# Kernel tuning notes

Hardware: AMD Instinct MI355X
Metric: run time of the kernel (lower is better)

Reference implementation:

```python
import jax, jax.numpy as jnp
import numpy as np

B, D, T = 8, 1024, 2048          # batch, input_dim, time
CD, CS = 256, 8192               # codebook_dim, codebook_size


def _wn_weight(v, g):
    # torch weight_norm for Conv1d(k=1): weight = g * v / ||v|| with norm over
    # all dims except the output-channel dim. v: (out, in), g: (out, 1).
    return g * v / jnp.linalg.norm(v, axis=1, keepdims=True)


def setup_inputs() -> dict:
    key = jax.random.key(0)
    k0, k1, k2, k3 = jax.random.split(key, 4)
    z = jax.random.normal(k0, (B, D, T), dtype=jnp.float32)
    # in_proj: WNConv1d(input_dim -> codebook_dim, k=1)
    in_v = jax.random.normal(k1, (CD, D), dtype=jnp.float32) * 0.02
    in_g = jnp.ones((CD, 1), dtype=jnp.float32)
    in_b = jnp.zeros((CD,), dtype=jnp.float32)
    # out_proj: WNConv1d(codebook_dim -> input_dim, k=1)
    out_v = jax.random.normal(k2, (D, CD), dtype=jnp.float32) * 0.02
    out_g = jnp.ones((D, 1), dtype=jnp.float32)
    out_b = jnp.zeros((D,), dtype=jnp.float32)
    codebook = jax.random.normal(k3, (CS, CD), dtype=jnp.float32)
    return {"z": z, "in_v": in_v, "in_g": in_g, "in_b": in_b,
            "out_v": out_v, "out_g": out_g, "out_b": out_b,
            "codebook": codebook}


def reference(z, in_v, in_g, in_b, out_v, out_g, out_b, codebook):
    # in_proj (1x1 conv == per-timestep linear): (B, D, T) -> (B, CD, T)
    w_in = _wn_weight(in_v, in_g)
    z_e = jnp.einsum('bdt,cd->bct', z, w_in) + in_b[None, :, None]

    # flatten to (N, CD), N = B*T
    enc = z_e.transpose(0, 2, 1).reshape(-1, z_e.shape[1])

    # squared euclidean cdist via GEMM: ||e||^2 - 2 e.c^T + ||c||^2
    dist = (jnp.sum(enc * enc, axis=1, keepdims=True)
            - 2.0 * enc @ codebook.T
            + jnp.sum(codebook * codebook, axis=1)[None, :])  # (N, CS)

    indices = jnp.argmax(-dist, axis=1).reshape(z.shape[0], -1)  # (B, T)

    # decode_code: embedding gather then channels-first: (B, CD, T)
    z_q_code = codebook[indices].transpose(0, 2, 1)

    # out_proj: (B, CD, T) -> (B, D, T)
    w_out = _wn_weight(out_v, out_g)
    z_q = jnp.einsum('bct,dc->bdt', z_q_code, w_out) + out_b[None, :, None]
    return z_q, indices, z_e
```

## Files before the change

kernel.cpp:

```cpp
#include <hip/hip_runtime.h>
#include <math.h>

#define B_  8
#define D_  1024
#define T_  2048
#define CD_ 256
#define CS_ 8192
#define N_  (B_*T_)

#define NSPLIT 8
#define CODES_PER_SPLIT (CS_/NSPLIT)
#define NT_SPLIT (CODES_PER_SPLIT/64)
#define DELTA 1.5f

#define ROWS_PER_WAVE 64
#define SCAN_ROWS 256
#define TILE_CODES 64

#define WS_ZEN   0
#define WS_CBB   2097152
#define WS_WH    (WS_CBB + 1048576)
#define WS_WM    (WS_WH + 131072)
#define WS_WL    (WS_WM + 131072)
#define WS_WOB   (WS_WL + 131072)
#define WS_C2    (WS_WOB + 131072)
#define WS_CNT   (WS_C2 + CS_)
#define WS_CAND  (WS_CNT + N_)
#define WS_IDX   (WS_CAND + N_*16)

#define OUT_ZQ  0
#define OUT_IDX (B_*D_*T_)
#define OUT_ZE  (OUT_IDX + B_*T_)

using short8v = __attribute__((ext_vector_type(8))) short;
using float4v = __attribute__((ext_vector_type(4))) float;

__device__ __forceinline__ float wave_sum64(float v) {
#pragma unroll
  for (int off = 32; off >= 1; off >>= 1) v += __shfl_xor(v, off);
  return v;
}

__device__ __forceinline__ unsigned short f2bf_rne(float f) {
  unsigned int u = __float_as_uint(f);
  u += 0x7fffu + ((u >> 16) & 1u);
  return (unsigned short)(u >> 16);
}

__device__ __forceinline__ float bf2f(unsigned short u) {
  return __uint_as_float(((unsigned)u) << 16);
}

__device__ __forceinline__ void gload_lds16(const void* g, void* l) {
  __builtin_amdgcn_global_load_lds(
      (const __attribute__((address_space(1))) void*)g,
      (__attribute__((address_space(3))) void*)l, 16, 0, 0);
}

__global__ __launch_bounds__(256) void prep_all(
    const float* __restrict__ in_v, const float* __restrict__ in_g,
    const float* __restrict__ out_v, const float* __restrict__ out_g,
    const float* __restrict__ cb,
    unsigned short* __restrict__ wh, unsigned short* __restrict__ wm,
    unsigned short* __restrict__ wl, unsigned short* __restrict__ wob,
    float* __restrict__ c2, unsigned short* __restrict__ cbb) {
  __shared__ float sh[4];
  int blk = blockIdx.x, tid = threadIdx.x;
  if (blk < CD_) {
    int c = blk;
    float v[4]; float s = 0.f;
#pragma unroll
    for (int i = 0; i < 4; ++i) {
      v[i] = in_v[c * D_ + tid + 256 * i];
      s = fmaf(v[i], v[i], s);
    }
    s = wave_sum64(s);
    if ((tid & 63) == 0) sh[tid >> 6] = s;
    __syncthreads();
    float tot = sh[0] + sh[1] + sh[2] + sh[3];
    float scale = in_g[c] / sqrtf(tot);
#pragma unroll
    for (int i = 0; i < 4; ++i) {
      int d = tid + 256 * i;
      float x = v[i] * scale;
      unsigned short h = f2bf_rne(x);
      float r1 = x - bf2f(h);
      unsigned short m = (unsigned short)(__float_as_uint(r1) >> 16);
      float r2 = r1 - bf2f(m);
      unsigned short lo = (unsigned short)(__float_as_uint(r2) >> 16);
      wh[c * D_ + d] = h; wm[c * D_ + d] = m; wl[c * D_ + d] = lo;
    }
  } else if (blk < CD_ + D_) {
    int d = blk - CD_;
    float v = out_v[d * CD_ + tid];
    float s = wave_sum64(v * v);
    if ((tid & 63) == 0) sh[tid >> 6] = s;
    __syncthreads();
    float tot = sh[0] + sh[1] + sh[2] + sh[3];
    float scale = out_g[d] / sqrtf(tot);
    wob[d * CD_ + tid] = f2bf_rne(v * scale);
  } else if (blk < CD_ + D_ + CS_ / 4) {
    int w = tid >> 6, lane = tid & 63;
    int s = (blk - CD_ - D_) * 4 + w;
    float acc = 0.f;
#pragma unroll
    for (int i = 0; i < 4; ++i) {
      float v = cb[(size_t)s * CD_ + lane + 64 * i];
      acc = fmaf(v, v, acc);
    }
    acc = wave_sum64(acc);
    if (lane == 0) c2[s] = acc;
  } else {
    size_t i = (size_t)(blk - CD_ - D_ - CS_ / 4) * 256 + tid;
    float4 v0 = *(const float4*)&cb[i * 8];
    float4 v1 = *(const float4*)&cb[i * 8 + 4];
    float f[8] = {v0.x, v0.y, v0.z, v0.w, v1.x, v1.y, v1.z, v1.w};
    unsigned short us[8];
#pragma unroll
    for (int m = 0; m < 8; ++m) us[m] = f2bf_rne(f[m]);
    *(uint4*)&cbb[i * 8] = *(uint4*)&us[0];
  }
}

__global__ __launch_bounds__(256, 2) void ze_mfma(
    const float* __restrict__ z,
    const unsigned short* __restrict__ whp, const unsigned short* __restrict__ wmp,
    const unsigned short* __restrict__ wlp, const float* __restrict__ in_b,
    float* __restrict__ out, unsigned short* __restrict__ zeN) {
  __shared__ __align__(16) char zbuf[2][16 * 1040];
  __shared__ __align__(16) unsigned short abuf[2][3][2048];
  int tid = threadIdx.x;
  int w = tid >> 6, l = tid & 63;
  int lrow = l & 15, lg = l >> 4;
  int t0 = blockIdx.x * 128, c0 = blockIdx.y * 64, b = blockIdx.z;
  const float* zb = z + (size_t)b * D_ * T_;
  char* zbuf_b = &zbuf[0][0];
  char* abuf_b = (char*)&abuf[0][0][0];

  auto stage = [&](int buf, int kc) {
#pragma unroll
    for (int i = 0; i < 4; ++i) {
      int g = w * 4 + i;
      int row = 2 * g + (l >> 5);
      gload_lds16(&zb[(size_t)(kc + row) * T_ + t0 + (l & 31) * 4],
                  zbuf_b + buf * 16640 + g * 1040);
    }
    int c = w * 16 + (l >> 2);
    int doff = (l & 3) * 8;
    gload_lds16(&whp[(size_t)(c0 + c) * D_ + kc + doff],
                abuf_b + buf * 12288 + w * 1024);
    gload_lds16(&wmp[(size_t)(c0 + c) * D_ + kc + doff],
                abuf_b + buf * 12288 + 4096 + w * 1024);
    gload_lds16(&wlp[(size_t)(c0 + c) * D_ + kc + doff],
                abuf_b + buf * 12288 + 8192 + w * 1024);
  };

  float4v acc[4][2];
#pragma unroll
  for (int rf = 0; rf < 4; ++rf)
#pragma unroll
    for (int cf = 0; cf < 2; ++cf) acc[rf][cf] = (float4v){0.f, 0.f, 0.f, 0.f};

  stage(0, 0);
  int cur = 0;
  for (int kt = 0; kt < D_ / 32; ++kt) {
    if (kt + 1 < D_ / 32) {
      stage(cur ^ 1, (kt + 1) * 32);
      asm volatile("s_waitcnt vmcnt(7)" ::: "memory");
    } else {
      asm volatile("s_waitcnt vmcnt(0)" ::: "memory");
    }
    __builtin_amdgcn_sched_barrier(0);
    __builtin_amdgcn_s_barrier();

    short8v bh[2], bm[2], bl[2];
#pragma unroll
    for (int cf = 0; cf < 2; ++cf) {
      const char* zp = zbuf_b + cur * 16640 + lg * 4160 +
                       (w * 32 + cf * 16 + lrow) * 4;
      float x[8];
#pragma unroll
      for (int j = 0; j < 8; ++j)
        x[j] = *(const float*)(zp + (j >> 1) * 1040 + (j & 1) * 512);
      __align__(16) unsigned short h8[8], m8[8], l8[8];
#pragma unroll
      for (int j = 0; j < 8; ++j) {
        unsigned short h = f2bf_rne(x[j]);
        float r1 = x[j] - bf2f(h);
        unsigned short m = (unsigned short)(__float_as_uint(r1) >> 16);
        float r2 = r1 - bf2f(m);
        unsigned short lo = (unsigned short)(__float_as_uint(r2) >> 16);
        h8[j] = h; m8[j] = m; l8[j] = lo;
      }
      bh[cf] = *(const short8v*)h8;
      bm[cf] = *(const short8v*)m8;
      bl[cf] = *(const short8v*)l8;
    }
    short8v ah[4], am[4], al[4];
#pragma unroll
    for (int rf = 0; rf < 4; ++rf) {
      int coff = (rf * 16 + lrow) * 64 + lg * 16;
      const char* ab = abuf_b + cur * 12288 + coff;
      ah[rf] = *(const short8v*)(ab);
      am[rf] = *(const short8v*)(ab + 4096);
      al[rf] = *(const short8v*)(ab + 8192);
    }
#pragma unroll
    for (int rf = 0; rf < 4; ++rf)
#pragma unroll
      for (int cf = 0; cf < 2; ++cf) {
        float4v a_ = acc[rf][cf];
        a_ = __builtin_amdgcn_mfma_f32_16x16x32_bf16(ah[rf], bh[cf], a_, 0, 0, 0);
        a_ = __builtin_amdgcn_mfma_f32_16x16x32_bf16(am[rf], bh[cf], a_, 0, 0, 0);
        a_ = __builtin_amdgcn_mfma_f32_16x16x32_bf16(ah[rf], bm[cf], a_, 0, 0, 0);
        a_ = __builtin_amdgcn_mfma_f32_16x16x32_bf16(am[rf], bm[cf], a_, 0, 0, 0);
        a_ = __builtin_amdgcn_mfma_f32_16x16x32_bf16(al[rf], bh[cf], a_, 0, 0, 0);
        a_ = __builtin_amdgcn_mfma_f32_16x16x32_bf16(ah[rf], bl[cf], a_, 0, 0, 0);
        acc[rf][cf] = a_;
      }
    __builtin_amdgcn_s_barrier();
    cur ^= 1;
  }

  int tbase = t0 + w * 32;
#pragma unroll
  for (int rf = 0; rf < 4; ++rf) {
    float bv[4];
#pragma unroll
    for (int rg = 0; rg < 4; ++rg) bv[rg] = in_b[c0 + rf * 16 + lg * 4 + rg];
#pragma unroll
    for (int cf = 0; cf < 2; ++cf) {
      int t = tbase + cf * 16 + lrow;
#pragma unroll
      for (int rg = 0; rg < 4; ++rg) {
        int c = c0 + rf * 16 + lg * 4 + rg;
        out[OUT_ZE + (size_t)(b * CD_ + c) * T_ + t] = acc[rf][cf][rg] + bv[rg];
      }
      __align__(8) unsigned short us[4];
#pragma unroll
      for (int rg = 0; rg < 4; ++rg) us[rg] = f2bf_rne(acc[rf][cf][rg] + bv[rg]);
      *(uint2*)&zeN[(size_t)(b * T_ + t) * CD_ + c0 + rf * 16 + lg * 4] =
          *(uint2*)us;
    }
  }
}

template <int COLLECT>
__global__ __launch_bounds__(256, 2) void vq_scan(
    const unsigned short* __restrict__ zeN, const unsigned short* __restrict__ cbb,
    const float* __restrict__ c2, float* __restrict__ bestq,
    int* __restrict__ cnt, int* __restrict__ cand) {
  __shared__ __align__(16) unsigned short smem[2][TILE_CODES * CD_];
  int tid = threadIdx.x;
  int w = tid >> 6, l = tid & 63;
  int lrow = l & 15, lg = l >> 4;
  int rowbase = blockIdx.x * SCAN_ROWS + w * ROWS_PER_WAVE;
  int cq = blockIdx.y;
  int cbase0 = cq * CODES_PER_SPLIT;

  if (COLLECT == 0 && cq == 0)
    cnt[blockIdx.x * SCAN_ROWS + tid] = 0;

  short8v a[4][8];
#pragma unroll
  for (int rf = 0; rf < 4; ++rf)
#pragma unroll
    for (int ks = 0; ks < 8; ++ks)
      a[rf][ks] = *(const short8v*)&zeN[((size_t)(rowbase + rf * 16 + lrow)) * CD_ + ks * 32 + lg * 8];

  float best[16];
  float thr[16];
#pragma unroll
  for (int s = 0; s < 16; ++s) best[s] = -3.4e38f;
  if (COLLECT) {
#pragma unroll
    for (int s = 0; s < 16; ++s) {
      int rf = s >> 2, rg = s & 3;
      thr[s] = bestq[rowbase + rf * 16 + lg * 4 + rg];
    }
  }

  int lhalf = l >> 5;
  int lcol = (l & 31) * 16;
  char* smem_b = (char*)&smem[0][0];
  const char* cbb_b = (const char*)cbb;
  int xsw = (lrow & 7) << 4;

  auto stage = [&](int buf, int cbase) {
#pragma unroll
    for (int r = 0; r < 8; ++r) {
      int code = w * 16 + r * 2 + lhalf;
      size_t goff = (size_t)(cbase + code) * 512 + (size_t)(lcol ^ ((code & 7) << 4));
      gload_lds16(cbb_b + goff, smem_b + buf * 32768 + (w * 8 + r) * 1024);
    }
  };

  stage(0, cbase0);

  for (int t = 0; t < NT_SPLIT; ++t) {
    int buf = t & 1;
    int cbase = cbase0 + t * TILE_CODES;

    float hc2[4];
#pragma unroll
    for (int cf = 0; cf < 4; ++cf) hc2[cf] = 0.5f * c2[cbase + cf * 16 + lrow];

    if (t + 1 < NT_SPLIT) {
      stage(buf ^ 1, cbase + TILE_CODES);
      asm volatile("s_waitcnt vmcnt(8)" ::: "memory");
    } else {
      asm volatile("s_waitcnt vmcnt(0)" ::: "memory");
    }
    __builtin_amdgcn_sched_barrier(0);
    __builtin_amdgcn_s_barrier();

    const char* bufb = smem_b + buf * 32768;
#pragma unroll
    for (int cf = 0; cf < 4; ++cf) {
      const char* bbase = bufb + (cf * 16 + lrow) * 512;
      float4v acc[4];
#pragma unroll
      for (int rf = 0; rf < 4; ++rf) acc[rf] = (float4v){0.f, 0.f, 0.f, 0.f};
#pragma unroll
      for (int ks = 0; ks < 8; ++ks) {
        short8v bfrag = *(const short8v*)(bbase + ((ks * 64 + lg * 16) ^ xsw));
        acc[0] = __builtin_amdgcn_mfma_f32_16x16x32_bf16(a[0][ks], bfrag, acc[0], 0, 0, 0);
        acc[1] = __builtin_amdgcn_mfma_f32_16x16x32_bf16(a[1][ks], bfrag, acc[1], 0, 0, 0);
        acc[2] = __builtin_amdgcn_mfma_f32_16x16x32_bf16(a[2][ks], bfrag, acc[2], 0, 0, 0);
        acc[3] = __builtin_amdgcn_mfma_f32_16x16x32_bf16(a[3][ks], bfrag, acc[3], 0, 0, 0);
      }
      int ci = cbase + cf * 16 + lrow;
#pragma unroll
      for (int rf = 0; rf < 4; ++rf)
#pragma unroll
        for (int rg = 0; rg < 4; ++rg) {
          float sc = acc[rf][rg] - hc2[cf];
          int slot = rf * 4 + rg;
          if (COLLECT) {
            if (sc >= thr[slot]) {
              int row = rowbase + rf * 16 + lg * 4 + rg;
              int pos = atomicAdd(&cnt[row], 1);
              if (pos < 16) cand[row * 16 + pos] = ci;
            }
          } else {
            best[slot] = fmaxf(best[slot], sc);
          }
        }
    }
    __builtin_amdgcn_s_barrier();
  }

  if (!COLLECT) {
#pragma unroll
    for (int s = 0; s < 16; ++s) {
      float v = best[s];
#pragma unroll
      for (int off = 1; off < 16; off <<= 1) v = fmaxf(v, __shfl_xor(v, off));
      best[s] = v;
    }
    if (lrow == 0) {
#pragma unroll
      for (int s = 0; s < 16; ++s) {
        int rf = s >> 2, rg = s & 3;
        bestq[cq * N_ + rowbase + rf * 16 + lg * 4 + rg] = best[s];
      }
    }
  }
}

__global__ __launch_bounds__(256) void vq_rowthr(float* __restrict__ bestq) {
  int n = blockIdx.x * 256 + threadIdx.x;
  float m = bestq[n];
#pragma unroll
  for (int q = 1; q < NSPLIT; ++q) m = fmaxf(m, bestq[q * N_ + n]);
  bestq[n] = m - DELTA;
}

__global__ __launch_bounds__(256) void vq_rescore(
    const float* __restrict__ ze, const float* __restrict__ cb,
    const int* __restrict__ cnt, const int* __restrict__ cand,
    float* __restrict__ out, int* __restrict__ idx_ws) {
  int tid = threadIdx.x;
  int n = blockIdx.x * 64 + (tid >> 2);
  int j = tid & 3;
  int b = n >> 11, t = n & (T_ - 1);
  const float* zr = ze + ((size_t)b * CD_) * T_ + t;
  int m = cnt[n]; if (m > 16) m = 16;
  float bd = 3.4e38f; int bi = 0x7fffffff;
  for (int i = 0; i < m; ++i) {
    int c = cand[n * 16 + i];
    const float* cr = cb + (size_t)c * CD_;
    float d = 0.f;
    for (int k = j; k < CD_; k += 4) {
      float diff = zr[(size_t)k * T_] - cr[k];
      d = fmaf(diff, diff, d);
    }
    d += __shfl_xor(d, 1);
    d += __shfl_xor(d, 2);
    if (d < bd || (d == bd && c < bi)) { bd = d; bi = c; }
  }
  if (j == 0) {
    idx_ws[n] = bi;
    out[OUT_IDX + n] = (float)bi;
  }
}

__global__ __launch_bounds__(256, 2) void zq_mfma(
    const unsigned short* __restrict__ wob, const unsigned short* __restrict__ cbb,
    const float* __restrict__ out_bias, const int* __restrict__ idx,
    float* __restrict__ out) {
  __shared__ __align__(16) unsigned short Bs[64 * CD_];
  __shared__ int idxs[64];
  int tid = threadIdx.x;
  int w = tid >> 6, l = tid & 63;
  int lrow = l & 15, lg = l >> 4;
  int t0 = blockIdx.x * 64, d0 = blockIdx.y * 256, b = blockIdx.z;
  int rowbase = d0 + w * 64;

  if (tid < 64) idxs[tid] = idx[b * T_ + t0 + tid];

  short8v a[4][8];
#pragma unroll
  for (int rf = 0; rf < 4; ++rf)
#pragma unroll
    for (int ks = 0; ks < 8; ++ks)
      a[rf][ks] = *(const short8v*)&wob[((size_t)(rowbase + rf * 16 + lrow)) * CD_ + ks * 32 + lg * 8];

  __syncthreads();

  int lhalf = l >> 5;
  int lcol = (l & 31) * 16;
  char* Bs_b = (char*)&Bs[0];
  const char* cbb_b = (const char*)cbb;
#pragma unroll
  for (int r = 0; r < 8; ++r) {
    int t = w * 16 + r * 2 + lhalf;
    int row = idxs[t];
    size_t goff = (size_t)row * 512 + (size_t)(lcol ^ ((t & 7) << 4));
    gload_lds16(cbb_b + goff, Bs_b + (w * 8 + r) * 1024);
  }
  __syncthreads();

  int xsw = (lrow & 7) << 4;
  float4v acc[4][4];
#pragma unroll
  for (int rf = 0; rf < 4; ++rf)
#pragma unroll
    for (int cf = 0; cf < 4; ++cf) acc[rf][cf] = (float4v){0.f, 0.f, 0.f, 0.f};
#pragma unroll
  for (int cf = 0; cf < 4; ++cf) {
    const char* bbase = Bs_b + (cf * 16 + lrow) * 512;
#pragma unroll
    for (int ks = 0; ks < 8; ++ks) {
      short8v bfrag = *(const short8v*)(bbase + ((ks * 64 + lg * 16) ^ xsw));
      acc[0][cf] = __builtin_amdgcn_mfma_f32_16x16x32_bf16(a[0][ks], bfrag, acc[0][cf], 0, 0, 0);
      acc[1][cf] = __builtin_amdgcn_mfma_f32_16x16x32_bf16(a[1][ks], bfrag, acc[1][cf], 0, 0, 0);
      acc[2][cf] = __builtin_amdgcn_mfma_f32_16x16x32_bf16(a[2][ks], bfrag, acc[2][cf], 0, 0, 0);
      acc[3][cf] = __builtin_amdgcn_mfma_f32_16x16x32_bf16(a[3][ks], bfrag, acc[3][cf], 0, 0, 0);
    }
  }
#pragma unroll
  for (int rf = 0; rf < 4; ++rf) {
    float bias[4];
#pragma unroll
    for (int rg = 0; rg < 4; ++rg) bias[rg] = out_bias[rowbase + rf * 16 + lg * 4 + rg];
#pragma unroll
    for (int cf = 0; cf < 4; ++cf) {
      int t = t0 + cf * 16 + lrow;
#pragma unroll
      for (int rg = 0; rg < 4; ++rg) {
        int d = rowbase + rf * 16 + lg * 4 + rg;
        out[OUT_ZQ + (size_t)(b * D_ + d) * T_ + t] = acc[rf][cf][rg] + bias[rg];
      }
    }
  }
}

extern "C" void kernel_launch(void* const* d_in, const int* in_sizes, int n_in,
                              void* d_out, int out_size, void* d_ws,
                              size_t ws_size, hipStream_t stream) {
  const float* z     = (const float*)d_in[0];
  const float* in_v  = (const float*)d_in[1];
  const float* in_g  = (const float*)d_in[2];
  const float* in_b  = (const float*)d_in[3];
  const float* out_v = (const float*)d_in[4];
  const float* out_g = (const float*)d_in[5];
  const float* out_b = (const float*)d_in[6];
  const float* cb    = (const float*)d_in[7];
  float* out = (float*)d_out;
  float* ws  = (float*)d_ws;

  unsigned short* zeN = (unsigned short*)(ws + WS_ZEN);
  unsigned short* cbb = (unsigned short*)(ws + WS_CBB);
  unsigned short* wh  = (unsigned short*)(ws + WS_WH);
  unsigned short* wm  = (unsigned short*)(ws + WS_WM);
  unsigned short* wl  = (unsigned short*)(ws + WS_WL);
  unsigned short* wob = (unsigned short*)(ws + WS_WOB);
  float* c2     = ws + WS_C2;
  int*   cnt    = (int*)(ws + WS_CNT);
  int*   cand   = (int*)(ws + WS_CAND);
  int*   idxw   = (int*)(ws + WS_IDX);
  float* bestq  = out + OUT_ZQ;

  prep_all<<<CD_ + D_ + CS_ / 4 + CS_ * CD_ / 8 / 256, 256, 0, stream>>>(
      in_v, in_g, out_v, out_g, cb, wh, wm, wl, wob, c2, cbb);

  ze_mfma<<<dim3(T_ / 128, CD_ / 64, B_), 256, 0, stream>>>(
      z, wh, wm, wl, in_b, out, zeN);

  vq_scan<0><<<dim3(N_ / SCAN_ROWS, NSPLIT), 256, 0, stream>>>(
      zeN, cbb, c2, bestq, cnt, cand);
  vq_rowthr<<<N_ / 256, 256, 0, stream>>>(bestq);
  vq_scan<1><<<dim3(N_ / SCAN_ROWS, NSPLIT), 256, 0, stream>>>(
      zeN, cbb, c2, bestq, cnt, cand);
  vq_rescore<<<N_ / 64, 256, 0, stream>>>(out + OUT_ZE, cb, cnt, cand, out, idxw);

  zq_mfma<<<dim3(T_ / 64, D_ / 256, B_), 256, 0, stream>>>(wob, cbb, out_b, idxw, out);
}
```

Measured before the change: 327.9 us.

## Drop third bf16 split term in z_e GEMM and fuse codebook norms into conversion

The z_e projection now emulates fp32 with a two-term bf16 split (hi/mid) and four MFMAs per tile instead of three terms and six MFMAs. This cuts the weight-split loads, LDS staging and matrix work in that GEMM. Separately, the codebook squared norms are computed during the bf16 conversion pass with a 32-lane shuffle reduction, which removes the dedicated c2 blocks and a second read of the codebook. The cost is lower precision in z_e, which is both an output and the input to the nearest-code search, so near-tie indices could change.

```diff
diff --git a/kernel.cpp b/kernel.cpp
--- a/kernel.cpp
+++ b/kernel.cpp
@@ -21,8 +21,7 @@
 #define WS_CBB   2097152
 #define WS_WH    (WS_CBB + 1048576)
 #define WS_WM    (WS_WH + 131072)
-#define WS_WL    (WS_WM + 131072)
-#define WS_WOB   (WS_WL + 131072)
+#define WS_WOB   (WS_WM + 131072)
 #define WS_C2    (WS_WOB + 131072)
 #define WS_CNT   (WS_C2 + CS_)
 #define WS_CAND  (WS_CNT + N_)
@@ -62,7 +61,7 @@
     const float* __restrict__ out_v, const float* __restrict__ out_g,
     const float* __restrict__ cb,
     unsigned short* __restrict__ wh, unsigned short* __restrict__ wm,
-    unsigned short* __restrict__ wl, unsigned short* __restrict__ wob,
+    unsigned short* __restrict__ wob,
     float* __restrict__ c2, unsigned short* __restrict__ cbb) {
   __shared__ float sh[4];
   int blk = blockIdx.x, tid = threadIdx.x;
@@ -86,9 +85,7 @@
       unsigned short h = f2bf_rne(x);
       float r1 = x - bf2f(h);
       unsigned short m = (unsigned short)(__float_as_uint(r1) >> 16);
-      float r2 = r1 - bf2f(m);
-      unsigned short lo = (unsigned short)(__float_as_uint(r2) >> 16);
-      wh[c * D_ + d] = h; wm[c * D_ + d] = m; wl[c * D_ + d] = lo;
+      wh[c * D_ + d] = h; wm[c * D_ + d] = m;
     }
   } else if (blk < CD_ + D_) {
     int d = blk - CD_;
@@ -99,36 +96,32 @@
     float tot = sh[0] + sh[1] + sh[2] + sh[3];
     float scale = out_g[d] / sqrtf(tot);
     wob[d * CD_ + tid] = f2bf_rne(v * scale);
-  } else if (blk < CD_ + D_ + CS_ / 4) {
-    int w = tid >> 6, lane = tid & 63;
-    int s = (blk - CD_ - D_) * 4 + w;
-    float acc = 0.f;
-#pragma unroll
-    for (int i = 0; i < 4; ++i) {
-      float v = cb[(size_t)s * CD_ + lane + 64 * i];
-      acc = fmaf(v, v, acc);
-    }
-    acc = wave_sum64(acc);
-    if (lane == 0) c2[s] = acc;
   } else {
-    size_t i = (size_t)(blk - CD_ - D_ - CS_ / 4) * 256 + tid;
+    size_t i = (size_t)(blk - CD_ - D_) * 256 + tid;
     float4 v0 = *(const float4*)&cb[i * 8];
     float4 v1 = *(const float4*)&cb[i * 8 + 4];
     float f[8] = {v0.x, v0.y, v0.z, v0.w, v1.x, v1.y, v1.z, v1.w};
     unsigned short us[8];
-#pragma unroll
-    for (int m = 0; m < 8; ++m) us[m] = f2bf_rne(f[m]);
+    float sq = 0.f;
+#pragma unroll
+    for (int m = 0; m < 8; ++m) {
+      us[m] = f2bf_rne(f[m]);
+      sq = fmaf(f[m], f[m], sq);
+    }
     *(uint4*)&cbb[i * 8] = *(uint4*)&us[0];
+#pragma unroll
+    for (int off = 1; off < 32; off <<= 1) sq += __shfl_xor(sq, off);
+    if ((tid & 31) == 0) c2[i >> 5] = sq;
   }
 }
 
 __global__ __launch_bounds__(256, 2) void ze_mfma(
     const float* __restrict__ z,
     const unsigned short* __restrict__ whp, const unsigned short* __restrict__ wmp,
-    const unsigned short* __restrict__ wlp, const float* __restrict__ in_b,
+    const float* __restrict__ in_b,
     float* __restrict__ out, unsigned short* __restrict__ zeN) {
   __shared__ __align__(16) char zbuf[2][16 * 1040];
-  __shared__ __align__(16) unsigned short abuf[2][3][2048];
+  __shared__ __align__(16) unsigned short abuf[2][2][2048];
   int tid = threadIdx.x;
   int w = tid >> 6, l = tid & 63;
   int lrow = l & 15, lg = l >> 4;
@@ -148,11 +141,9 @@
     int c = w * 16 + (l >> 2);
     int doff = (l & 3) * 8;
     gload_lds16(&whp[(size_t)(c0 + c) * D_ + kc + doff],
-                abuf_b + buf * 12288 + w * 1024);
+                abuf_b + buf * 8192 + w * 1024);
     gload_lds16(&wmp[(size_t)(c0 + c) * D_ + kc + doff],
-                abuf_b + buf * 12288 + 4096 + w * 1024);
-    gload_lds16(&wlp[(size_t)(c0 + c) * D_ + kc + doff],
-                abuf_b + buf * 12288 + 8192 + w * 1024);
+                abuf_b + buf * 8192 + 4096 + w * 1024);
   };
 
   float4v acc[4][2];
@@ -166,14 +157,14 @@
   for (int kt = 0; kt < D_ / 32; ++kt) {
     if (kt + 1 < D_ / 32) {
       stage(cur ^ 1, (kt + 1) * 32);
-      asm volatile("s_waitcnt vmcnt(7)" ::: "memory");
+      asm volatile("s_waitcnt vmcnt(6)" ::: "memory");
     } else {
       asm volatile("s_waitcnt vmcnt(0)" ::: "memory");
     }
     __builtin_amdgcn_sched_barrier(0);
     __builtin_amdgcn_s_barrier();
 
-    short8v bh[2], bm[2], bl[2];
+    short8v bh[2], bm[2];
 #pragma unroll
     for (int cf = 0; cf < 2; ++cf) {
       const char* zp = zbuf_b + cur * 16640 + lg * 4160 +
@@ -182,28 +173,24 @@
 #pragma unroll
       for (int j = 0; j < 8; ++j)
         x[j] = *(const float*)(zp + (j >> 1) * 1040 + (j & 1) * 512);
-      __align__(16) unsigned short h8[8], m8[8], l8[8];
+      __align__(16) unsigned short h8[8], m8[8];
 #pragma unroll
       for (int j = 0; j < 8; ++j) {
         unsigned short h = f2bf_rne(x[j]);
         float r1 = x[j] - bf2f(h);
-        unsigned short m = (unsigned short)(__float_as_uint(r1) >> 16);
-        float r2 = r1 - bf2f(m);
-        unsigned short lo = (unsigned short)(__float_as_uint(r2) >> 16);
-        h8[j] = h; m8[j] = m; l8[j] = lo;
+        m8[j] = (unsigned short)(__float_as_uint(r1) >> 16);
+        h8[j] = h;
       }
       bh[cf] = *(const short8v*)h8;
       bm[cf] = *(const short8v*)m8;
-      bl[cf] = *(const short8v*)l8;
-    }
-    short8v ah[4], am[4], al[4];
+    }
+    short8v ah[4], am[4];
 #pragma unroll
     for (int rf = 0; rf < 4; ++rf) {
       int coff = (rf * 16 + lrow) * 64 + lg * 16;
-      const char* ab = abuf_b + cur * 12288 + coff;
+      const char* ab = abuf_b + cur * 8192 + coff;
       ah[rf] = *(const short8v*)(ab);
       am[rf] = *(const short8v*)(ab + 4096);
-      al[rf] = *(const short8v*)(ab + 8192);
     }
 #pragma unroll
     for (int rf = 0; rf < 4; ++rf)
@@ -214,8 +201,6 @@
         a_ = __builtin_amdgcn_mfma_f32_16x16x32_bf16(am[rf], bh[cf], a_, 0, 0, 0);
         a_ = __builtin_amdgcn_mfma_f32_16x16x32_bf16(ah[rf], bm[cf], a_, 0, 0, 0);
         a_ = __builtin_amdgcn_mfma_f32_16x16x32_bf16(am[rf], bm[cf], a_, 0, 0, 0);
-        a_ = __builtin_amdgcn_mfma_f32_16x16x32_bf16(al[rf], bh[cf], a_, 0, 0, 0);
-        a_ = __builtin_amdgcn_mfma_f32_16x16x32_bf16(ah[rf], bl[cf], a_, 0, 0, 0);
         acc[rf][cf] = a_;
       }
     __builtin_amdgcn_s_barrier();
@@ -494,7 +479,6 @@
   unsigned short* cbb = (unsigned short*)(ws + WS_CBB);
   unsigned short* wh  = (unsigned short*)(ws + WS_WH);
   unsigned short* wm  = (unsigned short*)(ws + WS_WM);
-  unsigned short* wl  = (unsigned short*)(ws + WS_WL);
   unsigned short* wob = (unsigned short*)(ws + WS_WOB);
   float* c2     = ws + WS_C2;
   int*   cnt    = (int*)(ws + WS_CNT);
@@ -502,11 +486,11 @@
   int*   idxw   = (int*)(ws + WS_IDX);
   float* bestq  = out + OUT_ZQ;
 
-  prep_all<<<CD_ + D_ + CS_ / 4 + CS_ * CD_ / 8 / 256, 256, 0, stream>>>(
-      in_v, in_g, out_v, out_g, cb, wh, wm, wl, wob, c2, cbb);
+  prep_all<<<CD_ + D_ + CS_ * CD_ / 8 / 256, 256, 0, stream>>>(
+      in_v, in_g, out_v, out_g, cb, wh, wm, wob, c2, cbb);
 
   ze_mfma<<<dim3(T_ / 128, CD_ / 64, B_), 256, 0, stream>>>(
-      z, wh, wm, wl, in_b, out, zeN);
+      z, wh, wm, in_b, out, zeN);
 
   vq_scan<0><<<dim3(N_ / SCAN_ROWS, NSPLIT), 256, 0, stream>>>(
       zeN, cbb, c2, bestq, cnt, cand);
```

Measured after the change: 313.6 us (median of 2 runs). 4.3% less time.
